# Kernel optimization log

Measured on AMD Instinct MI355X. Metric: run time of the kernel, lower is better.

The kernel has to match this reference:

```python
import jax, jax.numpy as jnp
import numpy as np

N_NODES = 50000
N_EDGES = 800000
NUM_MOL = 2000
MSG_PASSES = 4


def setup_inputs() -> dict:
    key = jax.random.key(0)
    ks = jax.random.split(key, 16)
    x = jax.random.randint(ks[0], (N_NODES,), 0, 119)
    edge_attr = jax.random.randint(ks[1], (N_EDGES,), 0, 4)
    edge_index = jax.random.randint(ks[2], (2, N_EDGES), 0, N_NODES)
    batch = jnp.sort(jax.random.randint(ks[3], (N_NODES,), 0, NUM_MOL))
    f32 = jnp.float32
    return {
        "x": x,
        "edge_attr": edge_attr,
        "edge_index": edge_index,
        "batch": batch,
        "atom_table": jax.random.normal(ks[4], (119, 128), f32) * 0.1,
        "bond_table": jax.random.normal(ks[5], (4, 64), f32) * 0.1,
        "Wi": jax.random.normal(ks[6], (192, 128), f32) * 0.05,
        "bi": jax.random.normal(ks[7], (128,), f32) * 0.01,
        "Wu1": jax.random.normal(ks[8], (320, 128), f32) * 0.05,
        "bu1": jax.random.normal(ks[9], (128,), f32) * 0.01,
        "Wu2": jax.random.normal(ks[10], (128, 128), f32) * 0.05,
        "bu2": jax.random.normal(ks[11], (128,), f32) * 0.01,
        "Wr1": jax.random.normal(ks[12], (128, 512), f32) * 0.05,
        "br1": jax.random.normal(ks[13], (512,), f32) * 0.01,
        "Wr2": jax.random.normal(ks[14], (512, 1), f32) * 0.05,
        "br2": jax.random.normal(ks[15], (1,), f32) * 0.01,
    }


def reference(x, edge_attr, edge_index, batch,
              atom_table, bond_table, Wi, bi, Wu1, bu1, Wu2, bu2,
              Wr1, br1, Wr2, br2):
    atom = atom_table[x]                      # [N, atom_emb]
    bond = bond_table[edge_attr]              # [E, bond_emb]
    src, dst = edge_index[0], edge_index[1]
    a_src = atom[src]                         # [E, atom_emb]
    ab = jnp.concatenate([a_src, bond], axis=1)  # [E, atom_emb+bond_emb]
    msg = jax.nn.relu(ab @ Wi + bi)           # [E, msg_dim]
    for _ in range(MSG_PASSES):
        agg = jax.ops.segment_sum(msg, dst, num_segments=N_NODES)  # [N, msg_dim]
        upd_in = jnp.concatenate([ab, agg[src]], axis=1)           # [E, 320]
        h = jax.nn.relu(upd_in @ Wu1 + bu1)
        msg = jax.nn.relu(h @ Wu2 + bu2)
    node_state = jax.ops.segment_sum(msg, dst, num_segments=N_NODES)
    mol_state = jax.ops.segment_sum(node_state, batch, num_segments=NUM_MOL)
    out = jax.nn.relu(mol_state @ Wr1 + br1) @ Wr2 + br2  # [NUM_MOL, 1]
    return jnp.squeeze(out, axis=-1)
```

## Files before the change

kernel.cpp:

```cpp
#include <hip/hip_runtime.h>
#include <hip/hip_bf16.h>

#define N_NODES 50000
#define N_EDGES 800000
#define NUM_MOL 2000

typedef __attribute__((ext_vector_type(8))) short short8;
typedef __attribute__((ext_vector_type(4))) float f32x4;

union bfbits { __hip_bfloat16 b; short s; };

__global__ void k_tables(const float* __restrict__ atom_table,
                         const float* __restrict__ bond_table,
                         const float* __restrict__ Wi,
                         const float* __restrict__ bi,
                         const float* __restrict__ Wu1,
                         const float* __restrict__ bu1,
                         float* __restrict__ T1, float* __restrict__ U1,
                         float* __restrict__ T2c, float* __restrict__ U2c) {
  int b = blockIdx.x;
  int c = threadIdx.x;
  if (b < 119) {
    float t = 0.f, u = 0.f;
    for (int k = 0; k < 128; k++) {
      float a = atom_table[b * 128 + k];
      t += a * Wi[k * 128 + c];
      u += a * Wu1[k * 128 + c];
    }
    T1[b * 128 + c] = t;
    U1[b * 128 + c] = u;
  } else {
    int a = b - 119;
    float t = bi[c], u = bu1[c];
    for (int k = 0; k < 64; k++) {
      float bv = bond_table[a * 64 + k];
      t += bv * Wi[(128 + k) * 128 + c];
      u += bv * Wu1[(128 + k) * 128 + c];
    }
    T2c[a * 128 + c] = t;
    U2c[a * 128 + c] = u;
  }
}

__global__ void k_prep(const float* __restrict__ T1, const float* __restrict__ T2c,
                       const float* __restrict__ Wu2, const float* __restrict__ Wu1,
                       float* __restrict__ TT,
                       short* __restrict__ Wt, short* __restrict__ Wlo,
                       short* __restrict__ W1t, short* __restrict__ W1lo) {
  int b = blockIdx.x;
  int k = threadIdx.x;
  if (b < 476) {
    float v = T1[(b >> 2) * 128 + k] + T2c[(b & 3) * 128 + k];
    TT[b * 128 + k] = v > 0.f ? v : 0.f;
  } else if (b < 604) {
    int n = b - 476;
    float w = Wu2[k * 128 + n];
    bfbits hi; hi.b = __float2bfloat16(w);
    float hf = __bfloat162float(hi.b);
    bfbits lo; lo.b = __float2bfloat16(w - hf);
    Wt[n * 128 + k] = hi.s;
    Wlo[n * 128 + k] = lo.s;
  } else {
    int n = b - 604;
    float w = Wu1[(192 + k) * 128 + n];
    bfbits hi; hi.b = __float2bfloat16(w);
    float hf = __bfloat162float(hi.b);
    bfbits lo; lo.b = __float2bfloat16(w - hf);
    W1t[n * 128 + k] = hi.s;
    W1lo[n * 128 + k] = lo.s;
  }
}

__global__ void k_fillb(const int* __restrict__ eidx, const int* __restrict__ attr,
                        const int* __restrict__ x,
                        int* __restrict__ cnt, int* __restrict__ csr1) {
  int e = blockIdx.x * 256 + threadIdx.x;
  int d = eidx[N_EDGES + e];
  int s = eidx[e];
  int a = attr[e];
  int pos = atomicAdd(&cnt[d], 1);
  if (pos < 64) {
    int packed = (s * 4 + a) | ((x[s] * 4 + a) << 18);
    csr1[d * 64 + pos] = packed;
  }
}

__global__ void k_molptr(const int* __restrict__ batch, int* __restrict__ molptr) {
  int m = blockIdx.x * 256 + threadIdx.x;
  if (m > NUM_MOL) return;
  int lo = 0, hi = N_NODES;
  while (lo < hi) {
    int mid = (lo + hi) >> 1;
    if (batch[mid] < m) lo = mid + 1; else hi = mid;
  }
  molptr[m] = lo;
}

__global__ void k_gather0(const int* __restrict__ cnt, const int* __restrict__ csr1,
                          const float* __restrict__ TT, float* __restrict__ A_) {
  int n = blockIdx.x * 4 + (threadIdx.x >> 6);
  int lane = threadIdx.x & 63;
  int g = lane >> 5;
  int p = lane & 31;
  int beg = n * 64;
  int end = beg + cnt[n];
  float s0 = 0.f, s1 = 0.f, s2 = 0.f, s3 = 0.f;
  int i = beg;
  for (; i + 7 < end; i += 8) {
    int iA = ((unsigned)csr1[i + g]) >> 18;
    int iB = ((unsigned)csr1[i + 2 + g]) >> 18;
    int iC = ((unsigned)csr1[i + 4 + g]) >> 18;
    int iD = ((unsigned)csr1[i + 6 + g]) >> 18;
    float4 va = *(const float4*)&TT[iA * 128 + p * 4];
    float4 vb = *(const float4*)&TT[iB * 128 + p * 4];
    float4 vc = *(const float4*)&TT[iC * 128 + p * 4];
    float4 vd = *(const float4*)&TT[iD * 128 + p * 4];
    s0 += (va.x + vb.x) + (vc.x + vd.x);
    s1 += (va.y + vb.y) + (vc.y + vd.y);
    s2 += (va.z + vb.z) + (vc.z + vd.z);
    s3 += (va.w + vb.w) + (vc.w + vd.w);
  }
  for (; i + 3 < end; i += 4) {
    int iA = ((unsigned)csr1[i + g]) >> 18;
    int iB = ((unsigned)csr1[i + 2 + g]) >> 18;
    float4 va = *(const float4*)&TT[iA * 128 + p * 4];
    float4 vb = *(const float4*)&TT[iB * 128 + p * 4];
    s0 += va.x + vb.x; s1 += va.y + vb.y;
    s2 += va.z + vb.z; s3 += va.w + vb.w;
  }
  for (; i < end; i += 2) {
    if (i + g < end) {
      int idx = ((unsigned)csr1[i + g]) >> 18;
      float4 v = *(const float4*)&TT[idx * 128 + p * 4];
      s0 += v.x; s1 += v.y; s2 += v.z; s3 += v.w;
    }
  }
  s0 += __shfl_xor(s0, 32, 64);
  s1 += __shfl_xor(s1, 32, 64);
  s2 += __shfl_xor(s2, 32, 64);
  s3 += __shfl_xor(s3, 32, 64);
  float2 o;
  o.x = (g == 0) ? s0 : s2;
  o.y = (g == 0) ? s1 : s3;
  *(float2*)&A_[n * 128 + p * 4 + g * 2] = o;
}

__global__ void k_gather(const int* __restrict__ cnt, const int* __restrict__ csr1,
                         const __hip_bfloat16* __restrict__ M, float* __restrict__ A_) {
  int n = blockIdx.x * 4 + (threadIdx.x >> 6);
  int lane = threadIdx.x & 63;
  int g = lane >> 4;
  int p = lane & 15;
  int beg = n * 64;
  int end = beg + cnt[n];
  float s[8];
#pragma unroll
  for (int j = 0; j < 8; j++) s[j] = 0.f;
  const short* Ms = (const short*)M;
  int i = beg;
  for (; i + 15 < end; i += 16) {
    int iA = csr1[i + g] & 0x3FFFF;
    int iB = csr1[i + 4 + g] & 0x3FFFF;
    int iC = csr1[i + 8 + g] & 0x3FFFF;
    int iD = csr1[i + 12 + g] & 0x3FFFF;
    short8 va = *(const short8*)&Ms[iA * 128 + p * 8];
    short8 vb = *(const short8*)&Ms[iB * 128 + p * 8];
    short8 vc = *(const short8*)&Ms[iC * 128 + p * 8];
    short8 vd = *(const short8*)&Ms[iD * 128 + p * 8];
#pragma unroll
    for (int j = 0; j < 4; j++) {
      float2 fa = __bfloat1622float2(*(const __hip_bfloat162*)&((const short*)&va)[j * 2]);
      float2 fb = __bfloat1622float2(*(const __hip_bfloat162*)&((const short*)&vb)[j * 2]);
      float2 fc = __bfloat1622float2(*(const __hip_bfloat162*)&((const short*)&vc)[j * 2]);
      float2 fd = __bfloat1622float2(*(const __hip_bfloat162*)&((const short*)&vd)[j * 2]);
      s[j * 2] += (fa.x + fb.x) + (fc.x + fd.x);
      s[j * 2 + 1] += (fa.y + fb.y) + (fc.y + fd.y);
    }
  }
  for (; i + 7 < end; i += 8) {
    int iA = csr1[i + g] & 0x3FFFF;
    int iB = csr1[i + 4 + g] & 0x3FFFF;
    short8 va = *(const short8*)&Ms[iA * 128 + p * 8];
    short8 vb = *(const short8*)&Ms[iB * 128 + p * 8];
#pragma unroll
    for (int j = 0; j < 4; j++) {
      float2 fa = __bfloat1622float2(*(const __hip_bfloat162*)&((const short*)&va)[j * 2]);
      float2 fb = __bfloat1622float2(*(const __hip_bfloat162*)&((const short*)&vb)[j * 2]);
      s[j * 2] += fa.x + fb.x;
      s[j * 2 + 1] += fa.y + fb.y;
    }
  }
  for (; i < end; i += 4) {
    if (i + g < end) {
      int idx = csr1[i + g] & 0x3FFFF;
      short8 va = *(const short8*)&Ms[idx * 128 + p * 8];
#pragma unroll
      for (int j = 0; j < 4; j++) {
        float2 fa = __bfloat1622float2(*(const __hip_bfloat162*)&((const short*)&va)[j * 2]);
        s[j * 2] += fa.x;
        s[j * 2 + 1] += fa.y;
      }
    }
  }
#pragma unroll
  for (int j = 0; j < 8; j++) s[j] += __shfl_xor(s[j], 16, 64);
#pragma unroll
  for (int j = 0; j < 8; j++) s[j] += __shfl_xor(s[j], 32, 64);
  float2 o;
  o.x = s[g * 2];
  o.y = s[g * 2 + 1];
  *(float2*)&A_[n * 128 + p * 8 + g * 2] = o;
}

__global__ __launch_bounds__(256, 2) void k_mm1m(const float* __restrict__ A_,
                                                 const short* __restrict__ W1t,
                                                 const short* __restrict__ W1lo,
                                                 const int* __restrict__ x,
                                                 const float* __restrict__ U1,
                                                 float* __restrict__ B2_) {
  __shared__ float mbuf[4][16][68];
  int t = threadIdx.x;
  int lane = t & 63;
  int m = lane & 15;
  int quad = lane >> 4;
  int wslot = t >> 6;
  int w0 = blockIdx.x * 4 + wslot;
  int h = w0 & 1;

  short8 whi[4][4], wlo[4][4];
#pragma unroll
  for (int kc = 0; kc < 4; kc++)
#pragma unroll
    for (int nt = 0; nt < 4; nt++) {
      int n = h * 64 + nt * 16 + m;
      whi[kc][nt] = *(const short8*)&W1t[n * 128 + kc * 32 + quad * 8];
      wlo[kc][nt] = *(const short8*)&W1lo[n * 128 + kc * 32 + quad * 8];
    }

  for (int tid = w0; tid < 6250; tid += 4096) {
    int s = tid >> 1;
    int row = s * 16 + m;
    f32x4 acc[4];
#pragma unroll
    for (int nt = 0; nt < 4; nt++) acc[nt] = (f32x4){0.f, 0.f, 0.f, 0.f};

#pragma unroll
    for (int kc = 0; kc < 4; kc++) {
      int k0 = kc * 32 + quad * 8;
      short8 ahi, alo;
      {
        float av[8];
        *(float4*)&av[0] = *(const float4*)&A_[row * 128 + k0];
        *(float4*)&av[4] = *(const float4*)&A_[row * 128 + k0 + 4];
#pragma unroll
        for (int j = 0; j < 8; j++) {
          float hv = av[j];
          bfbits hi; hi.b = __float2bfloat16(hv);
          float hf = __bfloat162float(hi.b);
          bfbits lo; lo.b = __float2bfloat16(hv - hf);
          ahi[j] = hi.s;
          alo[j] = lo.s;
        }
      }
#pragma unroll
      for (int nt = 0; nt < 4; nt++) {
        acc[nt] = __builtin_amdgcn_mfma_f32_16x16x32_bf16(ahi, whi[kc][nt], acc[nt], 0, 0, 0);
        acc[nt] = __builtin_amdgcn_mfma_f32_16x16x32_bf16(alo, whi[kc][nt], acc[nt], 0, 0, 0);
        acc[nt] = __builtin_amdgcn_mfma_f32_16x16x32_bf16(ahi, wlo[kc][nt], acc[nt], 0, 0, 0);
      }
    }

#pragma unroll
    for (int nt = 0; nt < 4; nt++)
#pragma unroll
      for (int r = 0; r < 4; r++)
        mbuf[wslot][quad * 4 + r][nt * 16 + m] = acc[nt][r];
#pragma unroll
    for (int p = 0; p < 4; p++) {
      int c = p * 64 + lane;
      int rr = c >> 4;
      int qf = c & 15;
      int n = s * 16 + rr;
      int xn = x[n];
      float4 v = *(const float4*)&mbuf[wslot][rr][qf * 4];
      float4 d = *(const float4*)&U1[xn * 128 + h * 64 + qf * 4];
      v.x += d.x; v.y += d.y; v.z += d.z; v.w += d.w;
      *(float4*)&B2_[n * 128 + h * 64 + qf * 4] = v;
    }
  }
}

__global__ __launch_bounds__(256, 2) void k_mm2(const float* __restrict__ B2_,
                                                const float* __restrict__ U2c,
                                                const short* __restrict__ Wt,
                                                const short* __restrict__ Wlo,
                                                const float* __restrict__ bu2,
                                                __hip_bfloat16* __restrict__ M) {
  __shared__ short mbuf[4][16][68];
  int t = threadIdx.x;
  int lane = t & 63;
  int m = lane & 15;
  int quad = lane >> 4;
  int wslot = t >> 6;
  int w0 = blockIdx.x * 4 + wslot;
  int h = w0 & 1;

  short8 whi[4][4], wlo[4][4];
#pragma unroll
  for (int kc = 0; kc < 4; kc++)
#pragma unroll
    for (int nt = 0; nt < 4; nt++) {
      int n = h * 64 + nt * 16 + m;
      whi[kc][nt] = *(const short8*)&Wt[n * 128 + kc * 32 + quad * 8];
      wlo[kc][nt] = *(const short8*)&Wlo[n * 128 + kc * 32 + quad * 8];
    }
  float bias[4];
#pragma unroll
  for (int nt = 0; nt < 4; nt++) bias[nt] = bu2[h * 64 + nt * 16 + m];

  for (int tid = w0; tid < 25000; tid += 4096) {
    int s = tid >> 1;
    int node = s * 4 + (m >> 2);
    int attr = m & 3;
    f32x4 acc[4];
#pragma unroll
    for (int nt = 0; nt < 4; nt++) acc[nt] = (f32x4){0.f, 0.f, 0.f, 0.f};

#pragma unroll
    for (int kc = 0; kc < 4; kc++) {
      int k0 = kc * 32 + quad * 8;
      short8 ahi, alo;
      {
        float bba[8], u2a[8];
        *(float4*)&bba[0] = *(const float4*)&B2_[node * 128 + k0];
        *(float4*)&bba[4] = *(const float4*)&B2_[node * 128 + k0 + 4];
        *(float4*)&u2a[0] = *(const float4*)&U2c[attr * 128 + k0];
        *(float4*)&u2a[4] = *(const float4*)&U2c[attr * 128 + k0 + 4];
#pragma unroll
        for (int j = 0; j < 8; j++) {
          float hv = bba[j] + u2a[j];
          hv = hv > 0.f ? hv : 0.f;
          bfbits hi; hi.b = __float2bfloat16(hv);
          float hf = __bfloat162float(hi.b);
          bfbits lo; lo.b = __float2bfloat16(hv - hf);
          ahi[j] = hi.s;
          alo[j] = lo.s;
        }
      }
#pragma unroll
      for (int nt = 0; nt < 4; nt++) {
        acc[nt] = __builtin_amdgcn_mfma_f32_16x16x32_bf16(ahi, whi[kc][nt], acc[nt], 0, 0, 0);
        acc[nt] = __builtin_amdgcn_mfma_f32_16x16x32_bf16(alo, whi[kc][nt], acc[nt], 0, 0, 0);
        acc[nt] = __builtin_amdgcn_mfma_f32_16x16x32_bf16(ahi, wlo[kc][nt], acc[nt], 0, 0, 0);
      }
    }

#pragma unroll
    for (int nt = 0; nt < 4; nt++) {
#pragma unroll
      for (int r = 0; r < 4; r++) {
        float v = acc[nt][r] + bias[nt];
        v = v > 0.f ? v : 0.f;
        bfbits o; o.b = __float2bfloat16(v);
        mbuf[wslot][quad * 4 + r][nt * 16 + m] = o.s;
      }
    }
    {
      int rr = lane >> 2;
      int qq = lane & 3;
      short8 v = *(const short8*)&mbuf[wslot][rr][qq * 8];
      *(short8*)((short*)M + (s * 16 + rr) * 128 + h * 64 + qq * 8) = v;
      short8 v2 = *(const short8*)&mbuf[wslot][rr][(qq + 4) * 8];
      *(short8*)((short*)M + (s * 16 + rr) * 128 + h * 64 + (qq + 4) * 8) = v2;
    }
  }
}

__global__ void k_molgather(const float* __restrict__ A_, const int* __restrict__ molptr,
                            float* __restrict__ mol) {
  int m = blockIdx.x * 4 + (threadIdx.x >> 6);
  int lane = threadIdx.x & 63;
  int beg = molptr[m], end = molptr[m + 1];
  float ax = 0.f, ay = 0.f;
  int n = beg;
  for (; n + 1 < end; n += 2) {
    float2 v0 = *(const float2*)&A_[n * 128 + lane * 2];
    float2 v1 = *(const float2*)&A_[(n + 1) * 128 + lane * 2];
    ax += v0.x + v1.x;
    ay += v0.y + v1.y;
  }
  if (n < end) {
    float2 v0 = *(const float2*)&A_[n * 128 + lane * 2];
    ax += v0.x;
    ay += v0.y;
  }
  float2 o; o.x = ax; o.y = ay;
  *(float2*)&mol[m * 128 + lane * 2] = o;
}

__global__ __launch_bounds__(256) void k_readout(const float* __restrict__ mol,
                                                 const float* __restrict__ Wr1,
                                                 const float* __restrict__ br1,
                                                 const float* __restrict__ Wr2,
                                                 const float* __restrict__ br2,
                                                 float* __restrict__ out) {
  int m0 = blockIdx.x * 8;
  __shared__ float ms[8][128];
  __shared__ float red[32];
  int t = threadIdx.x;
  int lane = t & 63;
  int wave = t >> 6;
  for (int i = t; i < 1024; i += 256)
    ms[i >> 7][i & 127] = mol[m0 * 128 + i];
  __syncthreads();
  float part[8];
#pragma unroll
  for (int q = 0; q < 8; q++) part[q] = 0.f;
#pragma unroll
  for (int jj = 0; jj < 2; jj++) {
    int j = t + jj * 256;
    float b1 = br1[j];
    float acc[8];
#pragma unroll
    for (int q = 0; q < 8; q++) acc[q] = b1;
    for (int k = 0; k < 128; k += 4) {
      float4 w4 = *(const float4*)&Wr1[k * 512 + j];
      (void)w4;
      float w0 = Wr1[k * 512 + j];
      float w1 = Wr1[(k + 1) * 512 + j];
      float w2 = Wr1[(k + 2) * 512 + j];
      float w3 = Wr1[(k + 3) * 512 + j];
#pragma unroll
      for (int q = 0; q < 8; q++)
        acc[q] += ms[q][k] * w0 + ms[q][k + 1] * w1 + ms[q][k + 2] * w2 + ms[q][k + 3] * w3;
    }
    float w2v = Wr2[j];
#pragma unroll
    for (int q = 0; q < 8; q++) {
      float a = acc[q] > 0.f ? acc[q] : 0.f;
      part[q] += a * w2v;
    }
  }
#pragma unroll
  for (int q = 0; q < 8; q++) {
    float v = part[q];
    v += __shfl_xor(v, 32, 64);
    v += __shfl_xor(v, 16, 64);
    v += __shfl_xor(v, 8, 64);
    v += __shfl_xor(v, 4, 64);
    v += __shfl_xor(v, 2, 64);
    v += __shfl_xor(v, 1, 64);
    if (lane == 0) red[wave * 8 + q] = v;
  }
  __syncthreads();
  if (t < 8)
    out[m0 + t] = red[t] + red[8 + t] + red[16 + t] + red[24 + t] + br2[0];
}

extern "C" void kernel_launch(void* const* d_in, const int* in_sizes, int n_in,
                              void* d_out, int out_size, void* d_ws, size_t ws_size,
                              hipStream_t stream) {
  const int* x        = (const int*)d_in[0];
  const int* eattr    = (const int*)d_in[1];
  const int* eidx     = (const int*)d_in[2];
  const int* batch    = (const int*)d_in[3];
  const float* atom_table = (const float*)d_in[4];
  const float* bond_table = (const float*)d_in[5];
  const float* Wi  = (const float*)d_in[6];
  const float* bi  = (const float*)d_in[7];
  const float* Wu1 = (const float*)d_in[8];
  const float* bu1 = (const float*)d_in[9];
  const float* Wu2 = (const float*)d_in[10];
  const float* bu2 = (const float*)d_in[11];
  const float* Wr1 = (const float*)d_in[12];
  const float* br1 = (const float*)d_in[13];
  const float* Wr2 = (const float*)d_in[14];
  const float* br2 = (const float*)d_in[15];
  float* out = (float*)d_out;

  char* ws = (char*)d_ws;
  __hip_bfloat16* M = (__hip_bfloat16*)(ws);
  short* Wt      = (short*)(ws + 51200000);
  short* Wlo     = (short*)(ws + 51232768);
  short* W1t     = (short*)(ws + 51265536);
  short* W1lo    = (short*)(ws + 51298304);
  int*   molptr  = (int*)  (ws + 51331072);
  int*   cnt     = (int*)  (ws + 51340000);
  int*   csr1    = (int*)  (ws + 52000000);
  float* A       = (float*)(ws + 102400000);
  float* B2      = (float*)(ws + 128000000);
  float* T1      = (float*)(ws + 157000064);
  float* U1      = (float*)(ws + 157060992);
  float* T2c     = (float*)(ws + 157121920);
  float* U2c     = (float*)(ws + 157123968);
  float* TT      = (float*)(ws + 157126016);
  float* mol     = (float*)(ws + 157369728);

  hipMemsetAsync(cnt, 0, N_NODES * sizeof(int), stream);
  k_tables<<<123, 128, 0, stream>>>(atom_table, bond_table, Wi, bi, Wu1, bu1,
                                    T1, U1, T2c, U2c);
  k_prep<<<732, 128, 0, stream>>>(T1, T2c, Wu2, Wu1, TT, Wt, Wlo, W1t, W1lo);
  k_fillb<<<N_EDGES / 256, 256, 0, stream>>>(eidx, eattr, x, cnt, csr1);
  k_molptr<<<(NUM_MOL + 256) / 256, 256, 0, stream>>>(batch, molptr);

  k_gather0<<<N_NODES / 4, 256, 0, stream>>>(cnt, csr1, TT, A);

  for (int p = 0; p < 4; p++) {
    k_mm1m<<<1024, 256, 0, stream>>>(A, W1t, W1lo, x, U1, B2);
    k_mm2<<<1024, 256, 0, stream>>>(B2, U2c, Wt, Wlo, bu2, M);
    k_gather<<<N_NODES / 4, 256, 0, stream>>>(cnt, csr1, M, A);
  }

  k_molgather<<<NUM_MOL / 4, 256, 0, stream>>>(A, molptr, mol);
  k_readout<<<NUM_MOL / 8, 256, 0, stream>>>(mol, Wr1, br1, Wr2, br2, out);
}
```

Before: 620.0 us.

## Build CSR via two-pass binning to localize scattered writes

Result: slower. 637.6 us (+2.8%).

```diff
diff --git a/kernel.cpp b/kernel.cpp
--- a/kernel.cpp
+++ b/kernel.cpp
@@ -4,6 +4,9 @@
 #define N_NODES 50000
 #define N_EDGES 800000
 #define NUM_MOL 2000
+
+#define NBIN2 6250
+#define BCAP2 128
 
 typedef __attribute__((ext_vector_type(8))) short short8;
 typedef __attribute__((ext_vector_type(4))) float f32x4;
@@ -71,17 +74,32 @@
   }
 }
 
-__global__ void k_fillb(const int* __restrict__ eidx, const int* __restrict__ attr,
-                        const int* __restrict__ x,
-                        int* __restrict__ cnt, int* __restrict__ csr1) {
+__global__ void k_bin(const int* __restrict__ eidx, const int* __restrict__ attr,
+                      const int* __restrict__ x,
+                      int* __restrict__ bincnt, int2* __restrict__ bins) {
   int e = blockIdx.x * 256 + threadIdx.x;
+  int grp = blockIdx.x & 7;
   int d = eidx[N_EDGES + e];
   int s = eidx[e];
   int a = attr[e];
-  int pos = atomicAdd(&cnt[d], 1);
-  if (pos < 64) {
+  int bin = d >> 3;
+  int pos = atomicAdd(&bincnt[grp * NBIN2 + bin], 1);
+  if (pos < BCAP2) {
     int packed = (s * 4 + a) | ((x[s] * 4 + a) << 18);
-    csr1[d * 64 + pos] = packed;
+    bins[(grp * NBIN2 + bin) * BCAP2 + pos] = make_int2(packed, d);
+  }
+}
+
+__global__ void k_scatter(const int* __restrict__ bincnt, const int2* __restrict__ bins,
+                          int* __restrict__ cnt, int* __restrict__ csr1) {
+  int bin = blockIdx.x;
+  int grp = threadIdx.x >> 5;
+  int c = bincnt[grp * NBIN2 + bin];
+  if (c > BCAP2) c = BCAP2;
+  for (int i = threadIdx.x & 31; i < c; i += 32) {
+    int2 r = bins[(grp * NBIN2 + bin) * BCAP2 + i];
+    int pos = atomicAdd(&cnt[r.y], 1);
+    if (pos < 64) csr1[r.y * 64 + pos] = r.x;
   }
 }
 
@@ -424,8 +442,6 @@
 #pragma unroll
     for (int q = 0; q < 8; q++) acc[q] = b1;
     for (int k = 0; k < 128; k += 4) {
-      float4 w4 = *(const float4*)&Wr1[k * 512 + j];
-      (void)w4;
       float w0 = Wr1[k * 512 + j];
       float w1 = Wr1[(k + 1) * 512 + j];
       float w2 = Wr1[(k + 2) * 512 + j];
@@ -486,6 +502,7 @@
   short* W1lo    = (short*)(ws + 51298304);
   int*   molptr  = (int*)  (ws + 51331072);
   int*   cnt     = (int*)  (ws + 51340000);
+  int*   bincnt  = (int*)  (ws + 51540000);
   int*   csr1    = (int*)  (ws + 52000000);
   float* A       = (float*)(ws + 102400000);
   float* B2      = (float*)(ws + 128000000);
@@ -496,11 +513,15 @@
   float* TT      = (float*)(ws + 157126016);
   float* mol     = (float*)(ws + 157369728);
 
+  int2* bins = (int2*)(ws + 102400000);
+
   hipMemsetAsync(cnt, 0, N_NODES * sizeof(int), stream);
+  hipMemsetAsync(bincnt, 0, 8 * NBIN2 * sizeof(int), stream);
   k_tables<<<123, 128, 0, stream>>>(atom_table, bond_table, Wi, bi, Wu1, bu1,
                                     T1, U1, T2c, U2c);
   k_prep<<<732, 128, 0, stream>>>(T1, T2c, Wu2, Wu1, TT, Wt, Wlo, W1t, W1lo);
-  k_fillb<<<N_EDGES / 256, 256, 0, stream>>>(eidx, eattr, x, cnt, csr1);
+  k_bin<<<N_EDGES / 256, 256, 0, stream>>>(eidx, eattr, x, bincnt, bins);
+  k_scatter<<<NBIN2, 256, 0, stream>>>(bincnt, bins, cnt, csr1);
   k_molptr<<<(NUM_MOL + 256) / 256, 256, 0, stream>>>(batch, molptr);
 
   k_gather0<<<N_NODES / 4, 256, 0, stream>>>(cnt, csr1, TT, A);
```

## Reuse each B2 row across four bond attributes in mm2 tile

Applied to the files above, without the earlier changes.

New measurement: 802.7 us. +29.5%, slower.

```diff
diff --git a/kernel.cpp b/kernel.cpp
--- a/kernel.cpp
+++ b/kernel.cpp
@@ -318,24 +318,27 @@
 #pragma unroll
   for (int nt = 0; nt < 4; nt++) bias[nt] = bu2[h * 64 + nt * 16 + m];
 
-  for (int tid = w0; tid < 25000; tid += 4096) {
+  for (int tid = w0; tid < 6250; tid += 3128) {
     int s = tid >> 1;
-    int node = s * 4 + (m >> 2);
-    int attr = m & 3;
-    f32x4 acc[4];
-#pragma unroll
-    for (int nt = 0; nt < 4; nt++) acc[nt] = (f32x4){0.f, 0.f, 0.f, 0.f};
+    int row = s * 16 + m;
+    f32x4 acc[4][4];
+#pragma unroll
+    for (int a = 0; a < 4; a++)
+#pragma unroll
+      for (int nt = 0; nt < 4; nt++) acc[a][nt] = (f32x4){0.f, 0.f, 0.f, 0.f};
 
 #pragma unroll
     for (int kc = 0; kc < 4; kc++) {
       int k0 = kc * 32 + quad * 8;
-      short8 ahi, alo;
-      {
-        float bba[8], u2a[8];
-        *(float4*)&bba[0] = *(const float4*)&B2_[node * 128 + k0];
-        *(float4*)&bba[4] = *(const float4*)&B2_[node * 128 + k0 + 4];
-        *(float4*)&u2a[0] = *(const float4*)&U2c[attr * 128 + k0];
-        *(float4*)&u2a[4] = *(const float4*)&U2c[attr * 128 + k0 + 4];
+      float bba[8];
+      *(float4*)&bba[0] = *(const float4*)&B2_[row * 128 + k0];
+      *(float4*)&bba[4] = *(const float4*)&B2_[row * 128 + k0 + 4];
+#pragma unroll
+      for (int a = 0; a < 4; a++) {
+        float u2a[8];
+        *(float4*)&u2a[0] = *(const float4*)&U2c[a * 128 + k0];
+        *(float4*)&u2a[4] = *(const float4*)&U2c[a * 128 + k0 + 4];
+        short8 ahi, alo;
 #pragma unroll
         for (int j = 0; j < 8; j++) {
           float hv = bba[j] + u2a[j];
@@ -346,32 +349,36 @@
           ahi[j] = hi.s;
           alo[j] = lo.s;
         }
+#pragma unroll
+        for (int nt = 0; nt < 4; nt++) {
+          acc[a][nt] = __builtin_amdgcn_mfma_f32_16x16x32_bf16(ahi, whi[kc][nt], acc[a][nt], 0, 0, 0);
+          acc[a][nt] = __builtin_amdgcn_mfma_f32_16x16x32_bf16(alo, whi[kc][nt], acc[a][nt], 0, 0, 0);
+          acc[a][nt] = __builtin_amdgcn_mfma_f32_16x16x32_bf16(ahi, wlo[kc][nt], acc[a][nt], 0, 0, 0);
+        }
       }
+    }
+
+#pragma unroll
+    for (int a = 0; a < 4; a++) {
 #pragma unroll
       for (int nt = 0; nt < 4; nt++) {
-        acc[nt] = __builtin_amdgcn_mfma_f32_16x16x32_bf16(ahi, whi[kc][nt], acc[nt], 0, 0, 0);
-        acc[nt] = __builtin_amdgcn_mfma_f32_16x16x32_bf16(alo, whi[kc][nt], acc[nt], 0, 0, 0);
-        acc[nt] = __builtin_amdgcn_mfma_f32_16x16x32_bf16(ahi, wlo[kc][nt], acc[nt], 0, 0, 0);
+#pragma unroll
+        for (int r = 0; r < 4; r++) {
+          float v = acc[a][nt][r] + bias[nt];
+          v = v > 0.f ? v : 0.f;
+          bfbits o; o.b = __float2bfloat16(v);
+          mbuf[wslot][quad * 4 + r][nt * 16 + m] = o.s;
+        }
       }
-    }
-
-#pragma unroll
-    for (int nt = 0; nt < 4; nt++) {
-#pragma unroll
-      for (int r = 0; r < 4; r++) {
-        float v = acc[nt][r] + bias[nt];
-        v = v > 0.f ? v : 0.f;
-        bfbits o; o.b = __float2bfloat16(v);
-        mbuf[wslot][quad * 4 + r][nt * 16 + m] = o.s;
+      {
+        int rr = lane >> 2;
+        int qq = lane & 3;
+        long mrow = (long)((s * 16 + rr) * 4 + a);
+        short8 v = *(const short8*)&mbuf[wslot][rr][qq * 8];
+        *(short8*)((short*)M + mrow * 128 + h * 64 + qq * 8) = v;
+        short8 v2 = *(const short8*)&mbuf[wslot][rr][(qq + 4) * 8];
+        *(short8*)((short*)M + mrow * 128 + h * 64 + (qq + 4) * 8) = v2;
       }
-    }
-    {
-      int rr = lane >> 2;
-      int qq = lane & 3;
-      short8 v = *(const short8*)&mbuf[wslot][rr][qq * 8];
-      *(short8*)((short*)M + (s * 16 + rr) * 128 + h * 64 + qq * 8) = v;
-      short8 v2 = *(const short8*)&mbuf[wslot][rr][(qq + 4) * 8];
-      *(short8*)((short*)M + (s * 16 + rr) * 128 + h * 64 + (qq + 4) * 8) = v2;
     }
   }
 }
@@ -424,8 +431,6 @@
 #pragma unroll
     for (int q = 0; q < 8; q++) acc[q] = b1;
     for (int k = 0; k < 128; k += 4) {
-      float4 w4 = *(const float4*)&Wr1[k * 512 + j];
-      (void)w4;
       float w0 = Wr1[k * 512 + j];
       float w1 = Wr1[(k + 1) * 512 + j];
       float w2 = Wr1[(k + 2) * 512 + j];
@@ -507,7 +512,7 @@
 
   for (int p = 0; p < 4; p++) {
     k_mm1m<<<1024, 256, 0, stream>>>(A, W1t, W1lo, x, U1, B2);
-    k_mm2<<<1024, 256, 0, stream>>>(B2, U2c, Wt, Wlo, bu2, M);
+    k_mm2<<<782, 256, 0, stream>>>(B2, U2c, Wt, Wlo, bu2, M);
     k_gather<<<N_NODES / 4, 256, 0, stream>>>(cnt, csr1, M, A);
   }
 
```
